# Kernel tuning notes

Measured on AMD Instinct MI355X. Metric: run time of the kernel, lower is better.

The kernel has to match this reference:

```python
import jax, jax.numpy as jnp
import numpy as np

N = 10000
E = 320000


def spmm(edge_row, edge_col, edge_val, h):
    # out[i] = sum_{e: row[e]==i} val[e] * h[col[e]]  (sparse adjacency @ h)
    msgs = edge_val[:, None] * h[edge_col]          # [E, d]
    return jax.ops.segment_sum(msgs, edge_row, num_segments=N)


def setup_inputs() -> dict:
    key = jax.random.key(0)
    ks = jax.random.split(key, 8)
    x = jax.random.normal(ks[0], (N, 128), dtype=jnp.float32)
    edge_row = jax.random.randint(ks[1], (E,), 0, N, dtype=jnp.int32)
    edge_col = jax.random.randint(ks[2], (E,), 0, N, dtype=jnp.int32)
    edge_val = jax.random.uniform(ks[3], (E,), dtype=jnp.float32)
    # Xavier-uniform-ish init as in the torch module: U(-1/sqrt(fan_out), 1/sqrt(fan_out))
    def w(k, fi, fo):
        s = 1.0 / np.sqrt(fo)
        return jax.random.uniform(k, (fi, fo), minval=-s, maxval=s, dtype=jnp.float32)
    W0 = w(ks[4], 128, 128)
    W1 = w(ks[5], 128, 128)
    W2 = w(ks[6], 128, 64)
    Wb = w(ks[7], 64, 64)
    return {"x": x, "edge_row": edge_row, "edge_col": edge_col, "edge_val": edge_val,
            "W0": W0, "W1": W1, "W2": W2, "Wb": Wb}


def reference(x, edge_row, edge_col, edge_val, W0, W1, W2, Wb):
    h = x
    for W in (W0, W1, W2):
        h = jax.nn.elu(spmm(edge_row, edge_col, edge_val, h @ W))
        # dropout is inactive in eval mode (training=False)
    S = (Wb + Wb.T) * 0.5                          # symmetric [d, d]
    out = jax.nn.sigmoid(h @ (S @ h.T))            # [N, N]
    return out
```

## Files before the change

kernel.cpp:

```cpp
#include <hip/hip_runtime.h>
#include <hip/hip_bf16.h>
#include <math.h>

typedef short short8 __attribute__((ext_vector_type(8)));
typedef short short4v __attribute__((ext_vector_type(4)));
typedef float f32x4 __attribute__((ext_vector_type(4)));

__device__ inline void bsplit(float x, short& h, short& l) {
    __hip_bfloat16 hb = __float2bfloat16(x);
    float hf = __bfloat162float(hb);
    __hip_bfloat16 lb = __float2bfloat16(x - hf);
    h = *reinterpret_cast<short*>(&hb);
    l = *reinterpret_cast<short*>(&lb);
}


__global__ void zero_i32(int* __restrict__ p, int n) {
    int i = blockIdx.x * blockDim.x + threadIdx.x;
    if (i < n) p[i] = 0;
}

__global__ void hist_kernel(const int* __restrict__ row, int* __restrict__ hist, int E) {
    int i = blockIdx.x * blockDim.x + threadIdx.x;
    if (i < E) atomicAdd(&hist[row[i]], 1);
}

__global__ void scan_kernel(const int* __restrict__ hist, int* __restrict__ rowptr,
                            int* __restrict__ cursor, int n) {
    __shared__ int wsum[16];
    __shared__ int carry_s;
    int tid = threadIdx.x, lane = tid & 63, wid = tid >> 6;
    if (tid == 0) { carry_s = 0; rowptr[0] = 0; }
    __syncthreads();
    for (int base = 0; base < n; base += 1024) {
        int idx = base + tid;
        int v = (idx < n) ? hist[idx] : 0;
        int x = v;
#pragma unroll
        for (int d = 1; d < 64; d <<= 1) {
            int t = __shfl_up(x, d, 64);
            if (lane >= d) x += t;
        }
        if (lane == 63) wsum[wid] = x;
        __syncthreads();
        if (wid == 0) {
            int s = (lane < 16) ? wsum[lane] : 0;
#pragma unroll
            for (int d = 1; d < 16; d <<= 1) {
                int t = __shfl_up(s, d, 64);
                if (lane >= d) s += t;
            }
            if (lane < 16) wsum[lane] = s;
        }
        __syncthreads();
        int woff = (wid > 0) ? wsum[wid - 1] : 0;
        int inc = x + woff + carry_s;
        if (idx < n) {
            rowptr[idx + 1] = inc;
            cursor[idx] = inc - v;
        }
        __syncthreads();
        if (tid == 1023) carry_s = inc;
        __syncthreads();
    }
}

__global__ void scatter_kernel(const int* __restrict__ row, const int* __restrict__ col,
                               const float* __restrict__ val, int* __restrict__ cursor,
                               int* __restrict__ colsort, float* __restrict__ valsort, int E) {
    int i = blockIdx.x * blockDim.x + threadIdx.x;
    if (i < E) {
        int r = row[i];
        int p = atomicAdd(&cursor[r], 1);
        colsort[p] = col[i];
        valsort[p] = val[i];
    }
}

template <int K, int M>
__global__ void gemm_layer(const float* __restrict__ A, const float* __restrict__ W,
                           float* __restrict__ out, int n) {
    __shared__ float a[8 * K];
    int j = threadIdx.x;
    int row0 = blockIdx.x * 8;
    constexpr int K4 = K / 4;
    for (int idx = j; idx < 8 * K4; idx += M) {
        int r = idx / K4, k4 = idx % K4;
        float4 v = make_float4(0.f, 0.f, 0.f, 0.f);
        if (row0 + r < n) v = *reinterpret_cast<const float4*>(A + (long)(row0 + r) * K + k4 * 4);
        *reinterpret_cast<float4*>(a + r * K + k4 * 4) = v;
    }
    __syncthreads();
    float acc[8] = {0, 0, 0, 0, 0, 0, 0, 0};
#pragma unroll 8
    for (int k = 0; k < K; k++) {
        float w = W[k * M + j];
#pragma unroll
        for (int r = 0; r < 8; r++) acc[r] += a[r * K + k] * w;
    }
#pragma unroll
    for (int r = 0; r < 8; r++) {
        if (row0 + r < n) out[(long)(row0 + r) * M + j] = acc[r];
    }
}

__global__ void gemm_head(const float* __restrict__ A, const float* __restrict__ S,
                          short* __restrict__ Th, short* __restrict__ Tl, int n) {
    __shared__ float a[8 * 64];
    int j = threadIdx.x;
    int row0 = blockIdx.x * 8;
    for (int idx = j; idx < 8 * 16; idx += 64) {
        int r = idx >> 4, k4 = idx & 15;
        float4 v = make_float4(0.f, 0.f, 0.f, 0.f);
        if (row0 + r < n) v = *reinterpret_cast<const float4*>(A + (long)(row0 + r) * 64 + k4 * 4);
        *reinterpret_cast<float4*>(a + r * 64 + k4 * 4) = v;
    }
    __syncthreads();
    float acc[8] = {0, 0, 0, 0, 0, 0, 0, 0};
#pragma unroll 8
    for (int k = 0; k < 64; k++) {
        float w = S[k * 64 + j];
#pragma unroll
        for (int r = 0; r < 8; r++) acc[r] += a[r * 64 + k] * w;
    }
#pragma unroll
    for (int r = 0; r < 8; r++) {
        if (row0 + r < n) {
            short h, l;
            bsplit(acc[r], h, l);
            Th[(long)(row0 + r) * 64 + j] = h;
            Tl[(long)(row0 + r) * 64 + j] = l;
        }
    }
}

__global__ void spmm_elu_half(const int* __restrict__ rowptr, const int* __restrict__ cols,
                              const float* __restrict__ vals, const float* __restrict__ hw,
                              int tstride, float* __restrict__ out, int ostride, int n) {
    constexpr int LPR = 16, EPI = 4;
    int wave = (blockIdx.x * blockDim.x + threadIdx.x) >> 6;
    int lane = threadIdx.x & 63;
    if (wave >= n) return;
    int sub = lane % LPR, grp = lane / LPR;
    int s = rowptr[wave], e = rowptr[wave + 1];
    float ax = 0.f, ay = 0.f, az = 0.f, aw = 0.f;
    int pe = s + grp;
    int c = 0; float v = 0.f;
    if (pe < e) { c = cols[pe]; v = vals[pe]; }
    for (int p = s; p < e; p += EPI) {
        int pn = p + EPI + grp;
        int cn = 0; float vn = 0.f;
        if (pn < e) { cn = cols[pn]; vn = vals[pn]; }
        float4 h4 = *reinterpret_cast<const float4*>(hw + (long)c * tstride + sub * 4);
        ax += v * h4.x; ay += v * h4.y; az += v * h4.z; aw += v * h4.w;
        c = cn; v = vn;
    }
#pragma unroll
    for (int m = LPR; m < 64; m <<= 1) {
        ax += __shfl_xor(ax, m, 64);
        ay += __shfl_xor(ay, m, 64);
        az += __shfl_xor(az, m, 64);
        aw += __shfl_xor(aw, m, 64);
    }
    if (grp == 0) {
        float4 o;
        o.x = ax > 0.f ? ax : (__expf(ax) - 1.f);
        o.y = ay > 0.f ? ay : (__expf(ay) - 1.f);
        o.z = az > 0.f ? az : (__expf(az) - 1.f);
        o.w = aw > 0.f ? aw : (__expf(aw) - 1.f);
        *reinterpret_cast<float4*>(out + (long)wave * ostride + sub * 4) = o;
    }
}

__global__ void spmm_elu_split64(const int* __restrict__ rowptr, const int* __restrict__ cols,
                                 const float* __restrict__ vals, const float* __restrict__ hw,
                                 float* __restrict__ h3, short* __restrict__ Hh,
                                 short* __restrict__ Hl, int n) {
    constexpr int D = 64, LPR = 16, EPI = 4;
    int wave = (blockIdx.x * blockDim.x + threadIdx.x) >> 6;
    int lane = threadIdx.x & 63;
    if (wave >= n) return;
    int sub = lane % LPR, grp = lane / LPR;
    int s = rowptr[wave], e = rowptr[wave + 1];
    float ax = 0.f, ay = 0.f, az = 0.f, aw = 0.f;
    int pe = s + grp;
    int c = 0; float v = 0.f;
    if (pe < e) { c = cols[pe]; v = vals[pe]; }
    for (int p = s; p < e; p += EPI) {
        int pn = p + EPI + grp;
        int cn = 0; float vn = 0.f;
        if (pn < e) { cn = cols[pn]; vn = vals[pn]; }
        float4 h4 = *reinterpret_cast<const float4*>(hw + (long)c * D + sub * 4);
        ax += v * h4.x; ay += v * h4.y; az += v * h4.z; aw += v * h4.w;
        c = cn; v = vn;
    }
#pragma unroll
    for (int m = LPR; m < 64; m <<= 1) {
        ax += __shfl_xor(ax, m, 64);
        ay += __shfl_xor(ay, m, 64);
        az += __shfl_xor(az, m, 64);
        aw += __shfl_xor(aw, m, 64);
    }
    if (grp == 0) {
        float4 o;
        o.x = ax > 0.f ? ax : (__expf(ax) - 1.f);
        o.y = ay > 0.f ? ay : (__expf(ay) - 1.f);
        o.z = az > 0.f ? az : (__expf(az) - 1.f);
        o.w = aw > 0.f ? aw : (__expf(aw) - 1.f);
        *reinterpret_cast<float4*>(h3 + (long)wave * D + sub * 4) = o;
        short4v hs, ls;
        short t0, t1, t2, t3, u0, u1, u2, u3;
        bsplit(o.x, t0, u0);
        bsplit(o.y, t1, u1);
        bsplit(o.z, t2, u2);
        bsplit(o.w, t3, u3);
        hs[0] = t0; hs[1] = t1; hs[2] = t2; hs[3] = t3;
        ls[0] = u0; ls[1] = u1; ls[2] = u2; ls[3] = u3;
        *reinterpret_cast<short4v*>(Hh + (long)wave * D + sub * 4) = hs;
        *reinterpret_cast<short4v*>(Hl + (long)wave * D + sub * 4) = ls;
    }
}

__global__ void sym_kernel(const float* __restrict__ Wb, float* __restrict__ S) {
    int i = blockIdx.x * blockDim.x + threadIdx.x;
    if (i < 64 * 64) {
        int r = i >> 6, c = i & 63;
        S[i] = 0.5f * (Wb[r * 64 + c] + Wb[c * 64 + r]);
    }
}

__global__ void pad_zero(short* __restrict__ Th, short* __restrict__ Tl,
                         short* __restrict__ Hh, short* __restrict__ Hl,
                         int startRow, int padRows) {
    int i = blockIdx.x * blockDim.x + threadIdx.x;
    int tot = padRows * 64;
    if (i < tot) {
        long off = (long)startRow * 64 + i;
        Th[off] = 0; Tl[off] = 0; Hh[off] = 0; Hl[off] = 0;
    }
}

__global__ __launch_bounds__(256, 2) void final_mfma(
    const short* __restrict__ Th, const short* __restrict__ Tl,
    const short* __restrict__ Hh, const short* __restrict__ Hl,
    float* __restrict__ out, int n, int G, int ypx) {
    int bid = blockIdx.x;
    int xcd = bid & 7;
    int s4 = bid >> 3;
    int by = xcd * ypx + s4 % ypx;
    int bx = s4 / ypx;
    if (by >= G) return;

    int tid = threadIdx.x;
    int wave = tid >> 6, lane = tid & 63;
    int row0 = by * 128 + (wave >> 1) * 64;
    int col0 = bx * 128 + (wave & 1) * 64;
    int lrow = lane & 15;
    int koff = (lane >> 4) * 8;

    const short* ThB = Th + (long)(row0 + lrow) * 64 + koff;
    const short* TlB = Tl + (long)(row0 + lrow) * 64 + koff;
    const short* HhB = Hh + (long)(col0 + lrow) * 64 + koff;
    const short* HlB = Hl + (long)(col0 + lrow) * 64 + koff;

    f32x4 acc[4][4];
#pragma unroll
    for (int r = 0; r < 4; r++)
#pragma unroll
        for (int c = 0; c < 4; c++) acc[r][c] = (f32x4){0.f, 0.f, 0.f, 0.f};

#pragma unroll
    for (int ks = 0; ks < 2; ks++) {
        int kb = ks * 32;
        short8 ah[4], al[4];
#pragma unroll
        for (int r = 0; r < 4; r++) ah[r] = *reinterpret_cast<const short8*>(ThB + (long)(r * 16) * 64 + kb);
#pragma unroll
        for (int r = 0; r < 4; r++) al[r] = *reinterpret_cast<const short8*>(TlB + (long)(r * 16) * 64 + kb);

#pragma unroll
        for (int c = 0; c < 4; c++) {
            short8 bh = *reinterpret_cast<const short8*>(HhB + (long)(c * 16) * 64 + kb);
            short8 bl = *reinterpret_cast<const short8*>(HlB + (long)(c * 16) * 64 + kb);
#pragma unroll
            for (int r = 0; r < 4; r++)
                acc[r][c] = __builtin_amdgcn_mfma_f32_16x16x32_bf16(ah[r], bh, acc[r][c], 0, 0, 0);
#pragma unroll
            for (int r = 0; r < 4; r++)
                acc[r][c] = __builtin_amdgcn_mfma_f32_16x16x32_bf16(ah[r], bl, acc[r][c], 0, 0, 0);
#pragma unroll
            for (int r = 0; r < 4; r++)
                acc[r][c] = __builtin_amdgcn_mfma_f32_16x16x32_bf16(al[r], bh, acc[r][c], 0, 0, 0);
        }
    }

    int orow = (lane >> 4) * 4;
    bool full = (row0 + 64 <= n) && (col0 + 64 <= n);
    if (full) {
#pragma unroll
        for (int r = 0; r < 4; r++) {
#pragma unroll
            for (int q = 0; q < 4; q++) {
                long base = (long)(row0 + r * 16 + orow + q) * n + col0 + lrow;
#pragma unroll
                for (int c = 0; c < 4; c++) {
                    float x = acc[r][c][q];
                    __builtin_nontemporal_store(__builtin_amdgcn_rcpf(1.f + __expf(-x)),
                                                out + base + c * 16);
                }
            }
        }
    } else {
#pragma unroll
        for (int r = 0; r < 4; r++) {
#pragma unroll
            for (int q = 0; q < 4; q++) {
                int i = row0 + r * 16 + orow + q;
                if (i < n) {
#pragma unroll
                    for (int c = 0; c < 4; c++) {
                        int j = col0 + c * 16 + lrow;
                        if (j < n) {
                            float x = acc[r][c][q];
                            __builtin_nontemporal_store(__builtin_amdgcn_rcpf(1.f + __expf(-x)),
                                                        out + (long)i * n + j);
                        }
                    }
                }
            }
        }
    }
}

extern "C" void kernel_launch(void* const* d_in, const int* in_sizes, int n_in,
                              void* d_out, int out_size, void* d_ws, size_t ws_size,
                              hipStream_t stream) {
    const float* x    = (const float*)d_in[0];
    const int*   erow = (const int*)d_in[1];
    const int*   ecol = (const int*)d_in[2];
    const float* eval = (const float*)d_in[3];
    const float* W0   = (const float*)d_in[4];
    const float* W1   = (const float*)d_in[5];
    const float* W2   = (const float*)d_in[6];
    const float* Wb   = (const float*)d_in[7];
    float* out = (float*)d_out;

    int N = in_sizes[0] / 128;
    int E = in_sizes[1];
    int G = (N + 127) / 128;
    int Npad = G * 128;

    char* w = (char*)d_ws;
    size_t off = 0;
    auto alloc = [&](size_t bytes) -> void* {
        void* p = w + off;
        off += (bytes + 255) & ~(size_t)255;
        return p;
    };
    float* bufA    = (float*)alloc((size_t)N * 128 * 4);
    float* bufB    = (float*)alloc((size_t)N * 128 * 4);
    float* h3      = (float*)alloc((size_t)N * 64 * 4);
    float* S       = (float*)alloc(64 * 64 * 4);
    int*   colsort = (int*)alloc((size_t)E * 4);
    float* valsort = (float*)alloc((size_t)E * 4);
    int*   rowptr  = (int*)alloc((size_t)(N + 1) * 4);
    int*   cursor  = (int*)alloc((size_t)N * 4);
    int*   hist    = (int*)alloc((size_t)N * 4);
    short* Th      = (short*)alloc((size_t)Npad * 64 * 2);
    short* Tl      = (short*)alloc((size_t)Npad * 64 * 2);
    short* Hh      = (short*)alloc((size_t)Npad * 64 * 2);
    short* Hl      = (short*)alloc((size_t)Npad * 64 * 2);

    zero_i32<<<(N + 255) / 256, 256, 0, stream>>>(hist, N);
    hist_kernel<<<(E + 255) / 256, 256, 0, stream>>>(erow, hist, E);
    scan_kernel<<<1, 1024, 0, stream>>>(hist, rowptr, cursor, N);
    scatter_kernel<<<(E + 255) / 256, 256, 0, stream>>>(erow, ecol, eval, cursor, colsort, valsort, E);

    int gb8 = (N + 7) / 8;
    int spmmG = (N + 3) / 4;
    gemm_layer<128, 128><<<gb8, 128, 0, stream>>>(x, W0, bufB, N);
    spmm_elu_half<<<spmmG, 256, 0, stream>>>(rowptr, colsort, valsort, bufB, 128, bufA, 128, N);
    spmm_elu_half<<<spmmG, 256, 0, stream>>>(rowptr, colsort, valsort, bufB + 64, 128, bufA + 64, 128, N);
    gemm_layer<128, 128><<<gb8, 128, 0, stream>>>(bufA, W1, bufB, N);
    spmm_elu_half<<<spmmG, 256, 0, stream>>>(rowptr, colsort, valsort, bufB, 128, bufA, 128, N);
    spmm_elu_half<<<spmmG, 256, 0, stream>>>(rowptr, colsort, valsort, bufB + 64, 128, bufA + 64, 128, N);
    gemm_layer<128, 64><<<gb8, 64, 0, stream>>>(bufA, W2, bufB, N);
    spmm_elu_split64<<<spmmG, 256, 0, stream>>>(rowptr, colsort, valsort, bufB, h3, Hh, Hl, N);

    sym_kernel<<<16, 256, 0, stream>>>(Wb, S);
    gemm_head<<<gb8, 64, 0, stream>>>(h3, S, Th, Tl, N);

    int padRows = Npad - N;
    if (padRows > 0)
        pad_zero<<<(padRows * 64 + 255) / 256, 256, 0, stream>>>(Th, Tl, Hh, Hl, N, padRows);

    int ypx = (G + 7) / 8;
    int nwg = 8 * ypx * G;
    final_mfma<<<nwg, 256, 0, stream>>>(Th, Tl, Hh, Hl, out, N, G, ypx);
}
```

Baseline: 292.6 us.

## Merge half-width SpMM passes and fuse head GEMM into final SpMM

The two half-width SpMM launches per 128-wide layer become a single templated kernel in which each wave handles all 128 columns, using 32 lanes per row and 2 edges per iteration. The last SpMM now also computes the row's product with the symmetric matrix S through wave shuffles and writes the bf16 hi/lo split directly. This removes the h3 intermediate and the separate gemm_head launch. The trade-offs are 64 shuffles plus 64 global S loads per wave in the fused kernel, and fewer edges processed in parallel per wave in the 128-wide SpMM.

```diff
diff --git a/kernel.cpp b/kernel.cpp
--- a/kernel.cpp
+++ b/kernel.cpp
@@ -104,40 +104,12 @@
     }
 }
 
-__global__ void gemm_head(const float* __restrict__ A, const float* __restrict__ S,
-                          short* __restrict__ Th, short* __restrict__ Tl, int n) {
-    __shared__ float a[8 * 64];
-    int j = threadIdx.x;
-    int row0 = blockIdx.x * 8;
-    for (int idx = j; idx < 8 * 16; idx += 64) {
-        int r = idx >> 4, k4 = idx & 15;
-        float4 v = make_float4(0.f, 0.f, 0.f, 0.f);
-        if (row0 + r < n) v = *reinterpret_cast<const float4*>(A + (long)(row0 + r) * 64 + k4 * 4);
-        *reinterpret_cast<float4*>(a + r * 64 + k4 * 4) = v;
-    }
-    __syncthreads();
-    float acc[8] = {0, 0, 0, 0, 0, 0, 0, 0};
-#pragma unroll 8
-    for (int k = 0; k < 64; k++) {
-        float w = S[k * 64 + j];
-#pragma unroll
-        for (int r = 0; r < 8; r++) acc[r] += a[r * 64 + k] * w;
-    }
-#pragma unroll
-    for (int r = 0; r < 8; r++) {
-        if (row0 + r < n) {
-            short h, l;
-            bsplit(acc[r], h, l);
-            Th[(long)(row0 + r) * 64 + j] = h;
-            Tl[(long)(row0 + r) * 64 + j] = l;
-        }
-    }
-}
-
-__global__ void spmm_elu_half(const int* __restrict__ rowptr, const int* __restrict__ cols,
-                              const float* __restrict__ vals, const float* __restrict__ hw,
-                              int tstride, float* __restrict__ out, int ostride, int n) {
-    constexpr int LPR = 16, EPI = 4;
+template <int D>
+__global__ void spmm_elu_v2(const int* __restrict__ rowptr, const int* __restrict__ cols,
+                            const float* __restrict__ vals, const float* __restrict__ hw,
+                            float* __restrict__ out, int n) {
+    constexpr int LPR = D / 4;
+    constexpr int EPI = 64 / LPR;
     int wave = (blockIdx.x * blockDim.x + threadIdx.x) >> 6;
     int lane = threadIdx.x & 63;
     if (wave >= n) return;
@@ -151,7 +123,7 @@
         int pn = p + EPI + grp;
         int cn = 0; float vn = 0.f;
         if (pn < e) { cn = cols[pn]; vn = vals[pn]; }
-        float4 h4 = *reinterpret_cast<const float4*>(hw + (long)c * tstride + sub * 4);
+        float4 h4 = *reinterpret_cast<const float4*>(hw + (long)c * D + sub * 4);
         ax += v * h4.x; ay += v * h4.y; az += v * h4.z; aw += v * h4.w;
         c = cn; v = vn;
     }
@@ -168,14 +140,15 @@
         o.y = ay > 0.f ? ay : (__expf(ay) - 1.f);
         o.z = az > 0.f ? az : (__expf(az) - 1.f);
         o.w = aw > 0.f ? aw : (__expf(aw) - 1.f);
-        *reinterpret_cast<float4*>(out + (long)wave * ostride + sub * 4) = o;
-    }
-}
-
-__global__ void spmm_elu_split64(const int* __restrict__ rowptr, const int* __restrict__ cols,
-                                 const float* __restrict__ vals, const float* __restrict__ hw,
-                                 float* __restrict__ h3, short* __restrict__ Hh,
-                                 short* __restrict__ Hl, int n) {
+        *reinterpret_cast<float4*>(out + (long)wave * D + sub * 4) = o;
+    }
+}
+
+__global__ void spmm_fused3(const int* __restrict__ rowptr, const int* __restrict__ cols,
+                            const float* __restrict__ vals, const float* __restrict__ hw,
+                            const float* __restrict__ S,
+                            short* __restrict__ Hh, short* __restrict__ Hl,
+                            short* __restrict__ Th, short* __restrict__ Tl, int n) {
     constexpr int D = 64, LPR = 16, EPI = 4;
     int wave = (blockIdx.x * blockDim.x + threadIdx.x) >> 6;
     int lane = threadIdx.x & 63;
@@ -201,13 +174,13 @@
         az += __shfl_xor(az, m, 64);
         aw += __shfl_xor(aw, m, 64);
     }
+    float4 o;
+    o.x = ax > 0.f ? ax : (__expf(ax) - 1.f);
+    o.y = ay > 0.f ? ay : (__expf(ay) - 1.f);
+    o.z = az > 0.f ? az : (__expf(az) - 1.f);
+    o.w = aw > 0.f ? aw : (__expf(aw) - 1.f);
+
     if (grp == 0) {
-        float4 o;
-        o.x = ax > 0.f ? ax : (__expf(ax) - 1.f);
-        o.y = ay > 0.f ? ay : (__expf(ay) - 1.f);
-        o.z = az > 0.f ? az : (__expf(az) - 1.f);
-        o.w = aw > 0.f ? aw : (__expf(aw) - 1.f);
-        *reinterpret_cast<float4*>(h3 + (long)wave * D + sub * 4) = o;
         short4v hs, ls;
         short t0, t1, t2, t3, u0, u1, u2, u3;
         bsplit(o.x, t0, u0);
@@ -219,6 +192,23 @@
         *reinterpret_cast<short4v*>(Hh + (long)wave * D + sub * 4) = hs;
         *reinterpret_cast<short4v*>(Hl + (long)wave * D + sub * 4) = ls;
     }
+
+    float t = 0.f;
+#pragma unroll
+    for (int k = 0; k < 64; k++) {
+        float hk;
+        switch (k & 3) {
+            case 0: hk = __shfl(o.x, k >> 2, 64); break;
+            case 1: hk = __shfl(o.y, k >> 2, 64); break;
+            case 2: hk = __shfl(o.z, k >> 2, 64); break;
+            default: hk = __shfl(o.w, k >> 2, 64); break;
+        }
+        t += hk * S[k * 64 + lane];
+    }
+    short th, tl;
+    bsplit(t, th, tl);
+    Th[(long)wave * 64 + lane] = th;
+    Tl[(long)wave * 64 + lane] = tl;
 }
 
 __global__ void sym_kernel(const float* __restrict__ Wb, float* __restrict__ S) {
@@ -359,7 +349,6 @@
     };
     float* bufA    = (float*)alloc((size_t)N * 128 * 4);
     float* bufB    = (float*)alloc((size_t)N * 128 * 4);
-    float* h3      = (float*)alloc((size_t)N * 64 * 4);
     float* S       = (float*)alloc(64 * 64 * 4);
     int*   colsort = (int*)alloc((size_t)E * 4);
     float* valsort = (float*)alloc((size_t)E * 4);
@@ -378,17 +367,13 @@
 
     int gb8 = (N + 7) / 8;
     int spmmG = (N + 3) / 4;
+    sym_kernel<<<16, 256, 0, stream>>>(Wb, S);
     gemm_layer<128, 128><<<gb8, 128, 0, stream>>>(x, W0, bufB, N);
-    spmm_elu_half<<<spmmG, 256, 0, stream>>>(rowptr, colsort, valsort, bufB, 128, bufA, 128, N);
-    spmm_elu_half<<<spmmG, 256, 0, stream>>>(rowptr, colsort, valsort, bufB + 64, 128, bufA + 64, 128, N);
+    spmm_elu_v2<128><<<spmmG, 256, 0, stream>>>(rowptr, colsort, valsort, bufB, bufA, N);
     gemm_layer<128, 128><<<gb8, 128, 0, stream>>>(bufA, W1, bufB, N);
-    spmm_elu_half<<<spmmG, 256, 0, stream>>>(rowptr, colsort, valsort, bufB, 128, bufA, 128, N);
-    spmm_elu_half<<<spmmG, 256, 0, stream>>>(rowptr, colsort, valsort, bufB + 64, 128, bufA + 64, 128, N);
+    spmm_elu_v2<128><<<spmmG, 256, 0, stream>>>(rowptr, colsort, valsort, bufB, bufA, N);
     gemm_layer<128, 64><<<gb8, 64, 0, stream>>>(bufA, W2, bufB, N);
-    spmm_elu_split64<<<spmmG, 256, 0, stream>>>(rowptr, colsort, valsort, bufB, h3, Hh, Hl, N);
-
-    sym_kernel<<<16, 256, 0, stream>>>(Wb, S);
-    gemm_head<<<gb8, 64, 0, stream>>>(h3, S, Th, Tl, N);
+    spmm_fused3<<<spmmG, 256, 0, stream>>>(rowptr, colsort, valsort, bufB, S, Hh, Hl, Th, Tl, N);
 
     int padRows = Npad - N;
     if (padRows > 0)
```

Result: no change. 293.5 us (+0.3%).
